# Performance work log

Hardware: AMD Instinct MI355X
Metric: run time of the kernel (lower is better)

Reference implementation:

```python
import jax, jax.numpy as jnp
import numpy as np
from jax import lax

# --- static config (Detectron defaults, C4-style RPN) ---
B, A_NUM, H, W = 8, 15, 100, 168
STRIDE = 8.0                 # 1.0 / spatial_scale
PRE_NMS = 2000               # RPN_PRE_NMS_TOP_N
POST_NMS = 1000              # RPN_POST_NMS_TOP_N
NMS_THRESH = 0.7
MIN_SIZE = 0.0
BBOX_XFORM_CLIP = float(np.log(1000.0 / 16.0))


def _make_anchors():
    sizes = np.array([32., 64., 128., 256., 512.])
    ratios = np.array([0.5, 1.0, 2.0])
    out = []
    for s in sizes:
        for r in ratios:
            w = s * np.sqrt(1.0 / r)
            h = s * np.sqrt(r)
            out.append([-(w - 1) / 2., -(h - 1) / 2., (w - 1) / 2., (h - 1) / 2.])
    return np.asarray(out, dtype=np.float32)  # [15, 4]


def setup_inputs() -> dict:
    key = jax.random.key(0)
    k1, k2 = jax.random.split(key)
    rpn_cls_prob = jax.random.uniform(k1, (B, A_NUM, H, W), jnp.float32)
    rpn_bbox_pred = jax.random.normal(k2, (B, 4 * A_NUM, H, W), jnp.float32) * 0.1
    im_info = jnp.tile(jnp.array([[H * STRIDE, W * STRIDE, 1.0]], jnp.float32), (B, 1))
    anchors = jnp.asarray(_make_anchors())
    return {"rpn_cls_prob": rpn_cls_prob, "rpn_bbox_pred": rpn_bbox_pred,
            "im_info": im_info, "anchors": anchors}


def _bbox_transform(anchors, deltas):
    # Detectron bbox_transform with weights (1,1,1,1)
    ws = anchors[:, 2] - anchors[:, 0] + 1.0
    hs = anchors[:, 3] - anchors[:, 1] + 1.0
    cx = anchors[:, 0] + 0.5 * ws
    cy = anchors[:, 1] + 0.5 * hs
    dx, dy = deltas[:, 0], deltas[:, 1]
    dw = jnp.minimum(deltas[:, 2], BBOX_XFORM_CLIP)
    dh = jnp.minimum(deltas[:, 3], BBOX_XFORM_CLIP)
    pcx = dx * ws + cx
    pcy = dy * hs + cy
    pw = jnp.exp(dw) * ws
    ph = jnp.exp(dh) * hs
    return jnp.stack([pcx - 0.5 * pw, pcy - 0.5 * ph,
                      pcx + 0.5 * pw - 1.0, pcy + 0.5 * ph - 1.0], axis=1)


def _nms_keep(boxes, valid, thresh):
    # Greedy NMS on score-sorted boxes, fixed-shape via lax.scan.
    P = boxes.shape[0]
    x1, y1, x2, y2 = boxes[:, 0], boxes[:, 1], boxes[:, 2], boxes[:, 3]
    areas = (x2 - x1 + 1.0) * (y2 - y1 + 1.0)
    iw = jnp.maximum(jnp.minimum(x2[:, None], x2[None, :]) - jnp.maximum(x1[:, None], x1[None, :]) + 1.0, 0.0)
    ih = jnp.maximum(jnp.minimum(y2[:, None], y2[None, :]) - jnp.maximum(y1[:, None], y1[None, :]) + 1.0, 0.0)
    inter = iw * ih
    iou = inter / (areas[:, None] + areas[None, :] - inter)  # [P, P]
    idxs = jnp.arange(P)

    def step(suppressed, inp):
        row, is_valid, i = inp
        keep_i = is_valid & (~suppressed[i])
        suppressed = suppressed | (keep_i & (row > thresh) & (idxs > i))
        return suppressed, keep_i

    _, keep = lax.scan(step, jnp.zeros((P,), bool), (iou, valid, idxs))
    return keep


def _one_image(scores, deltas, iminfo, all_anchors):
    # scores: [A,H,W], deltas: [4A,H,W] -> flat (h, w, a) ordering, matching
    # all_anchors built as (K, A) with K = h*W + w.
    scores_f = jnp.transpose(scores, (1, 2, 0)).reshape(-1)          # [K*A]
    deltas_f = jnp.transpose(deltas, (1, 2, 0)).reshape(-1, 4)       # [K*A, 4]
    top_s, top_i = lax.top_k(scores_f, PRE_NMS)
    props = _bbox_transform(all_anchors[top_i], deltas_f[top_i])
    # clip_tiled_boxes to image bounds
    wmax, hmax = iminfo[1] - 1.0, iminfo[0] - 1.0
    x1 = jnp.clip(props[:, 0], 0.0, wmax)
    y1 = jnp.clip(props[:, 1], 0.0, hmax)
    x2 = jnp.clip(props[:, 2], 0.0, wmax)
    y2 = jnp.clip(props[:, 3], 0.0, hmax)
    props = jnp.stack([x1, y1, x2, y2], axis=1)
    # _filter_boxes (mask instead of drop, for fixed shapes)
    ws = x2 - x1 + 1.0
    hs = y2 - y1 + 1.0
    ms = MIN_SIZE * iminfo[2]
    valid = (ws >= ms) & (hs >= ms) & ((x1 + ws / 2.0) < iminfo[1]) & ((y1 + hs / 2.0) < iminfo[0])
    keep = _nms_keep(props, valid, NMS_THRESH)
    # kept boxes first (stable sort preserves descending-score order), take POST_NMS
    order = jnp.argsort(jnp.where(keep, 0, 1).astype(jnp.int32))[:POST_NMS]
    kept = keep[order]
    boxes = jnp.where(kept[:, None], props[order], 0.0)
    probs = jnp.where(kept, top_s[order], 0.0)
    return boxes, probs


def reference(rpn_cls_prob, rpn_bbox_pred, im_info, anchors):
    shift_x = jnp.arange(W, dtype=jnp.float32) * STRIDE
    shift_y = jnp.arange(H, dtype=jnp.float32) * STRIDE
    sx, sy = jnp.meshgrid(shift_x, shift_y)                 # [H, W] each
    shifts = jnp.stack([sx.ravel(), sy.ravel(), sx.ravel(), sy.ravel()], axis=1)  # [K, 4]
    all_anchors = (anchors[None, :, :] + shifts[:, None, :]).reshape(-1, 4)       # [K*A, 4]
    boxes, probs = jax.vmap(_one_image, in_axes=(0, 0, 0, None))(
        rpn_cls_prob, rpn_bbox_pred, im_info, all_anchors)      # [B,P,4], [B,P]
    binds = jnp.broadcast_to(jnp.arange(B, dtype=jnp.float32)[:, None, None], (B, POST_NMS, 1))
    rois = jnp.concatenate([binds, boxes], axis=2).reshape(B * POST_NMS, 5)
    return rois, probs.reshape(-1)
```

## Files before the change

### kernel.cpp

```cpp
#include <hip/hip_runtime.h>
#include <hip/hip_bf16.h>
#include <math.h>

#define BN 8
#define AN 15
#define HH 100
#define WW 168
#define HW (HH*WW)
#define NPI (AN*HW)
#define NTOT (BN*NPI)
#define PRE 2000
#define POST 1000
#define CAP 4096
#define ROWW 32
#define NCHUNK 32
#define RSTRIDE 2048
#define EPB 4096
#define HBLK 62
#define GELEM 2048
#define GBLK 124

typedef unsigned int u32;
typedef unsigned long long u64;

#define OFF_H1     0
#define OFF_H2     507904
#define OFF_CSTAR  1015808
#define OFF_CCNT   1016832
#define OFF_THR    1017856
#define OFF_CAND   1018880
#define OFF_BOX    1281024
#define OFF_SCORE  1543168
#define OFF_VALID  1608704
#define OFF_MASK   1674240
#define OFF_DIAG   5868544

__device__ __forceinline__ u32 fmono(float s) {
  u32 u = __float_as_uint(s);
  return (u & 0x80000000u) ? ~u : (u | 0x80000000u);
}
__device__ __forceinline__ float funmono(u32 m) {
  u32 u = (m & 0x80000000u) ? (m ^ 0x80000000u) : ~m;
  return __uint_as_float(u);
}
__device__ __forceinline__ float areaf(float4 bx) {
  return __fmul_rn(__fadd_rn(__fsub_rn(bx.z, bx.x), 1.0f),
                   __fadd_rn(__fsub_rn(bx.w, bx.y), 1.0f));
}

#define BAR_LGKM() asm volatile("s_waitcnt lgkmcnt(0)\ns_barrier" ::: "memory")
#define WAVE_FENCE() asm volatile("" ::: "memory")

__device__ __forceinline__ u32 wave_suffix_incl(u32 v, int lane) {
  for (int d = 1; d < 64; d <<= 1) {
    u32 n = (u32)__shfl_down((int)v, d, 64);
    if (lane + d < 64) v += n;
  }
  return v;
}

__global__ __launch_bounds__(256) void hist1_kernel(const float* __restrict__ cls,
                                                    u32* __restrict__ h1) {
  __shared__ u32 lh[16 * 258];
  int b = blockIdx.y;
  int t = threadIdx.x;
  for (int q = t; q < 16 * 258; q += 256) lh[q] = 0u;
  __syncthreads();
  int start = blockIdx.x * EPB;
  int end = min(start + EPB, NPI);
  const float* p = cls + (size_t)b * NPI;
  u32 copy = ((u32)t & 15u) * 258u;
  for (int i = start + t; i < end; i += 256) {
    u32 m = fmono(p[i]);
    atomicAdd(&lh[copy + (m >> 24)], 1u);
  }
  __syncthreads();
  u32 s = 0;
#pragma unroll
  for (int cpy = 0; cpy < 16; ++cpy) s += lh[cpy * 258 + t];
  h1[((size_t)(b * HBLK) + blockIdx.x) * 256 + t] = s;
}

__global__ __launch_bounds__(256) void coarse_kernel(const u32* __restrict__ h1,
                                                     u32* __restrict__ cstar) {
  int b = blockIdx.x;
  int t = threadIdx.x;
  __shared__ u32 cnts[256];
  u32 s = 0;
  for (int blk = 0; blk < HBLK; ++blk) s += h1[((size_t)(b * HBLK) + blk) * 256 + t];
  cnts[t] = s;
  __syncthreads();
  if (t < 64) {
    int lane = t;
    u32 v0 = cnts[4 * lane + 0], v1 = cnts[4 * lane + 1];
    u32 v2 = cnts[4 * lane + 2], v3 = cnts[4 * lane + 3];
    u32 ls3 = v3, ls2 = v2 + ls3, ls1 = v1 + ls2, ls0 = v0 + ls1;
    u32 incl = wave_suffix_incl(ls0, lane);
    u32 tail = incl - ls0;
    u32 s0 = tail + ls0, s1 = tail + ls1, s2 = tail + ls2, s3 = tail + ls3;
    u32 e0 = 4 * (u32)lane;
    if (lane == 0 && s0 < (u32)PRE) { cstar[b * 32] = 0u; cstar[b * 32 + 1] = s1; }
    if (s0 >= (u32)PRE && s1 < (u32)PRE) { cstar[b * 32] = e0 + 0; cstar[b * 32 + 1] = s1; }
    if (s1 >= (u32)PRE && s2 < (u32)PRE) { cstar[b * 32] = e0 + 1; cstar[b * 32 + 1] = s2; }
    if (s2 >= (u32)PRE && s3 < (u32)PRE) { cstar[b * 32] = e0 + 2; cstar[b * 32 + 1] = s3; }
    if (s3 >= (u32)PRE && (e0 + 3 == 255u || tail < (u32)PRE)) {
      cstar[b * 32] = e0 + 3;
      cstar[b * 32 + 1] = (e0 + 3 == 255u) ? 0u : tail;
    }
  }
}

__global__ __launch_bounds__(256) void hist2_kernel(const float* __restrict__ cls,
                                                    const u32* __restrict__ cstar,
                                                    u32* __restrict__ h2) {
  __shared__ u32 lh[4 * 260];
  int b = blockIdx.y;
  int t = threadIdx.x;
  for (int q = t; q < 4 * 260; q += 256) lh[q] = 0u;
  __syncthreads();
  u32 cs = cstar[b * 32];
  int start = blockIdx.x * EPB;
  int end = min(start + EPB, NPI);
  const float* p = cls + (size_t)b * NPI;
  u32 copy = ((u32)t & 3u) * 260u;
  for (int i = start + t; i < end; i += 256) {
    u32 m = fmono(p[i]);
    if ((m >> 24) == cs) atomicAdd(&lh[copy + ((m >> 16) & 0xFFu)], 1u);
  }
  __syncthreads();
  u32 s = 0;
#pragma unroll
  for (int cpy = 0; cpy < 4; ++cpy) s += lh[cpy * 260 + t];
  h2[((size_t)(b * HBLK) + blockIdx.x) * 256 + t] = s;
}

__global__ __launch_bounds__(256) void fine_kernel(const u32* __restrict__ h2,
                                                   const u32* __restrict__ cstar,
                                                   u32* __restrict__ thr,
                                                   u32* __restrict__ ccnt) {
  int b = blockIdx.x;
  int t = threadIdx.x;
  __shared__ u32 cnts[256];
  u32 s = 0;
  for (int blk = 0; blk < HBLK; ++blk) s += h2[((size_t)(b * HBLK) + blk) * 256 + t];
  cnts[t] = s;
  __syncthreads();
  if (t == 64) ccnt[b * 32] = 0u;
  if (t < 64) {
    int lane = t;
    u32 cs = cstar[b * 32], base = cstar[b * 32 + 1];
    u32 v0 = cnts[4 * lane + 0], v1 = cnts[4 * lane + 1];
    u32 v2 = cnts[4 * lane + 2], v3 = cnts[4 * lane + 3];
    u32 ls3 = v3, ls2 = v2 + ls3, ls1 = v1 + ls2, ls0 = v0 + ls1;
    u32 incl = wave_suffix_incl(ls0, lane);
    u32 tail = incl - ls0;
    u32 s0 = base + tail + ls0, s1 = base + tail + ls1;
    u32 s2 = base + tail + ls2, s3 = base + tail + ls3;
    u32 sn = base + tail;
    u32 e0 = 4 * (u32)lane;
    if (lane == 0 && s0 < (u32)PRE) thr[b * 32] = (cs << 8);
    if (s0 >= (u32)PRE && s1 < (u32)PRE) thr[b * 32] = (cs << 8) | (e0 + 0);
    if (s1 >= (u32)PRE && s2 < (u32)PRE) thr[b * 32] = (cs << 8) | (e0 + 1);
    if (s2 >= (u32)PRE && s3 < (u32)PRE) thr[b * 32] = (cs << 8) | (e0 + 2);
    if (s3 >= (u32)PRE && (e0 + 3 == 255u || sn < (u32)PRE)) thr[b * 32] = (cs << 8) | (e0 + 3);
  }
}

__global__ __launch_bounds__(256) void gather_kernel(
    const float* __restrict__ cls, const u32* __restrict__ thr,
    u32* __restrict__ ccnt, u64* __restrict__ cand) {
  int b = blockIdx.y;
  int t = threadIdx.x;
  int lane = t & 63, wid = t >> 6;
  int base_i = blockIdx.x * GELEM;
  const float* p = cls + (size_t)b * NPI;
  u32 T = thr[b * 32];
  __shared__ int wsum[4];
  __shared__ int wbase[4];
  __shared__ u32 baseSh;

  u32 mv[8];
  u32 flags = 0;
#pragma unroll
  for (int k = 0; k < 8; ++k) {
    int i = base_i + k * 256 + t;
    u32 m = 0;
    bool ok = false;
    if (i < NPI) { m = fmono(p[i]); ok = (m >> 16) >= T; }
    mv[k] = m;
    flags |= ok ? (1u << k) : 0u;
  }
  int ct = (int)__popc(flags);
  int inc = ct;
  for (int d = 1; d < 64; d <<= 1) {
    int n = __shfl_up(inc, d, 64);
    if (lane >= d) inc += n;
  }
  int excl = inc - ct;
  if (lane == 63) wsum[wid] = inc;
  __syncthreads();
  if (t == 0) {
    int acc = 0;
#pragma unroll
    for (int w = 0; w < 4; ++w) { wbase[w] = acc; acc += wsum[w]; }
    baseSh = acc ? atomicAdd(&ccnt[b * 32], (u32)acc) : 0u;
  }
  __syncthreads();
  if (!flags) return;
  u32 pos0 = baseSh + (u32)wbase[wid] + (u32)excl;
#pragma unroll
  for (int k = 0; k < 8; ++k) {
    if ((flags >> k) & 1u) {
      u32 pos = pos0 + (u32)__popc(flags & ((1u << k) - 1u));
      if (pos < CAP) {
        int i = base_i + k * 256 + t;
        int a = i / HW;
        int hw = i - a * HW;
        u32 ti = (u32)(hw * AN + a);
        cand[(size_t)b * CAP + pos] = ((u64)mv[k] << 32) | (u32)(~ti);
      }
    }
  }
}

__global__ __launch_bounds__(1024) void sort_transform_kernel(
    const u64* __restrict__ cand, const u32* __restrict__ ccnt,
    const u32* __restrict__ thr,
    const float* __restrict__ bbox, const float* __restrict__ iminfo,
    const float* __restrict__ anch,
    float4* __restrict__ boxes, float* __restrict__ scores, int* __restrict__ valid) {
  __shared__ u64 keys[CAP];
  __shared__ u64 keys2[2048];
  __shared__ u32 h24[256];
  __shared__ u32 aboveSh, cmpCnt, t24Sh, cnt2Sh;
  int b = blockIdx.x;
  int t = threadIdx.x;
  int lane = t & 63;
  u32 cnt = ccnt[b * 32];
  if (cnt > CAP) cnt = CAP;
  u32 thr16v = thr[b * 32];
  for (int q = t; q < CAP; q += 1024) keys[q] = (q < (int)cnt) ? cand[(size_t)b * CAP + q] : 0ULL;
  keys2[t] = 0ULL; keys2[t + 1024] = 0ULL;
  if (t < 256) h24[t] = 0u;
  if (t == 0) { aboveSh = 0u; cmpCnt = 0u; }
  __syncthreads();

  for (int q0 = 0; q0 < CAP; q0 += 1024) {
    int q = q0 + t;
    u64 key = keys[q];
    u32 hi = (u32)(key >> 32);
    bool isReal = (q < (int)cnt);
    bool above = isReal && ((hi >> 16) > thr16v);
    u64 bal = __ballot(above);
    if (lane == 0 && bal) atomicAdd(&aboveSh, (u32)__popcll(bal));
    if (isReal && !above) atomicAdd(&h24[(hi >> 8) & 0xFFu], 1u);
  }
  __syncthreads();
  if (t < 64) {
    u32 basev = aboveSh;
    u32 v0 = h24[4 * lane + 0], v1 = h24[4 * lane + 1];
    u32 v2 = h24[4 * lane + 2], v3 = h24[4 * lane + 3];
    u32 ls3 = v3, ls2 = v2 + ls3, ls1 = v1 + ls2, ls0 = v0 + ls1;
    u32 incl = wave_suffix_incl(ls0, lane);
    u32 tail = incl - ls0;
    u32 s0 = basev + tail + ls0, s1 = basev + tail + ls1;
    u32 s2 = basev + tail + ls2, s3 = basev + tail + ls3;
    u32 sn = basev + tail;
    u32 e0 = 4 * (u32)lane;
    if (lane == 0 && s0 < (u32)PRE) { t24Sh = 0u; cnt2Sh = s0; }
    if (s0 >= (u32)PRE && s1 < (u32)PRE) { t24Sh = e0 + 0; cnt2Sh = s0; }
    if (s1 >= (u32)PRE && s2 < (u32)PRE) { t24Sh = e0 + 1; cnt2Sh = s1; }
    if (s2 >= (u32)PRE && s3 < (u32)PRE) { t24Sh = e0 + 2; cnt2Sh = s2; }
    if (s3 >= (u32)PRE && (e0 + 3 == 255u || sn < (u32)PRE)) { t24Sh = e0 + 3; cnt2Sh = s3; }
  }
  __syncthreads();
  u32 cnt2 = cnt2Sh;
  bool fallback = (cnt2 > 2048u);

  if (!fallback) {
    u32 t24 = (thr16v << 8) | t24Sh;
    for (int q0 = 0; q0 < CAP; q0 += 1024) {
      int q = q0 + t;
      u64 key = keys[q];
      u32 hi = (u32)(key >> 32);
      bool pass = (q < (int)cnt) && ((hi >> 8) >= t24);
      u64 bal = __ballot(pass);
      if (bal) {
        u32 wb = 0;
        if (lane == 0) wb = atomicAdd(&cmpCnt, (u32)__popcll(bal));
        wb = (u32)__shfl((int)wb, 0, 64);
        if (pass) {
          u32 rank = (u32)__popcll(bal & ((1ULL << lane) - 1ULL));
          keys2[wb + rank] = key;
        }
      }
    }
    __syncthreads();
    for (u32 k = 2; k <= 2048; k <<= 1) {
      for (u32 j = k >> 1; j > 0; j >>= 1) {
        bool cross = (j >= 128);
        if (cross) __syncthreads();
        u32 idx = (u32)t;
        u32 base2 = ((idx & ~(j - 1)) << 1) | (idx & (j - 1));
        u32 partner = base2 + j;
        bool up2 = ((base2 & k) == 0);
        u64 A = keys2[base2], Bv = keys2[partner];
        bool sw = up2 ? (A < Bv) : (A > Bv);
        if (sw) { keys2[base2] = Bv; keys2[partner] = A; }
        if (cross) { if (j == 128) __syncthreads(); }
        else WAVE_FENCE();
      }
    }
    __syncthreads();
  } else {
    for (u32 k = 2; k <= CAP; k <<= 1) {
      for (u32 j = k >> 1; j > 0; j >>= 1) {
        for (int p = 0; p < CAP / 2 / 1024; ++p) {
          u32 idx = (u32)t + (u32)p * 1024u;
          u32 base2 = ((idx & ~(j - 1)) << 1) | (idx & (j - 1));
          u32 partner = base2 + j;
          bool up2 = ((base2 & k) == 0);
          u64 A = keys[base2], Bv = keys[partner];
          bool sw = up2 ? (A < Bv) : (A > Bv);
          if (sw) { keys[base2] = Bv; keys[partner] = A; }
        }
        __syncthreads();
      }
    }
  }

  float im_h = iminfo[b * 3 + 0], im_w = iminfo[b * 3 + 1], im_s = iminfo[b * 3 + 2];
  float wmax = __fsub_rn(im_w, 1.0f), hmax = __fsub_rn(im_h, 1.0f);
  float msz = __fmul_rn(0.0f, im_s);
  const float BCLIP = (float)4.135166556742356;
  for (int q = t; q < PRE; q += 1024) {
    u64 key = fallback ? keys[q] : keys2[q];
    u32 i = ~((u32)key);
    if (q >= (int)cnt || i >= (u32)NPI) {
      boxes[b * RSTRIDE + q] = make_float4(0.f, 0.f, 0.f, 0.f);
      scores[b * RSTRIDE + q] = 0.f;
      valid[b * RSTRIDE + q] = 0;
      continue;
    }
    float sc = funmono((u32)(key >> 32));
    int a = (int)(i % AN);
    int pp = (int)(i / AN);
    int w = pp % WW;
    int h = pp / WW;
    float sx = (float)(w * 8), sy = (float)(h * 8);
    float ax1 = __fadd_rn(anch[a * 4 + 0], sx);
    float ay1 = __fadd_rn(anch[a * 4 + 1], sy);
    float ax2 = __fadd_rn(anch[a * 4 + 2], sx);
    float ay2 = __fadd_rn(anch[a * 4 + 3], sy);
    float wsA = __fadd_rn(__fsub_rn(ax2, ax1), 1.0f);
    float hsA = __fadd_rn(__fsub_rn(ay2, ay1), 1.0f);
    float cx = __fadd_rn(ax1, __fmul_rn(0.5f, wsA));
    float cy = __fadd_rn(ay1, __fmul_rn(0.5f, hsA));
    const float* dp = bbox + ((size_t)b * (4 * AN) + 4 * a) * HW + (size_t)h * WW + w;
    float dx = dp[0], dy = dp[HW], dwv = dp[2 * HW], dhv = dp[3 * HW];
    dwv = fminf(dwv, BCLIP);
    dhv = fminf(dhv, BCLIP);
    float pcx = __fadd_rn(__fmul_rn(dx, wsA), cx);
    float pcy = __fadd_rn(__fmul_rn(dy, hsA), cy);
    float pw = __fmul_rn((float)exp((double)dwv), wsA);
    float ph = __fmul_rn((float)exp((double)dhv), hsA);
    float hpw = __fmul_rn(0.5f, pw), hph = __fmul_rn(0.5f, ph);
    float x1 = __fsub_rn(pcx, hpw);
    float y1 = __fsub_rn(pcy, hph);
    float x2 = __fsub_rn(__fadd_rn(pcx, hpw), 1.0f);
    float y2 = __fsub_rn(__fadd_rn(pcy, hph), 1.0f);
    x1 = fminf(fmaxf(x1, 0.0f), wmax);
    y1 = fminf(fmaxf(y1, 0.0f), hmax);
    x2 = fminf(fmaxf(x2, 0.0f), wmax);
    y2 = fminf(fmaxf(y2, 0.0f), hmax);
    float ws2 = __fadd_rn(__fsub_rn(x2, x1), 1.0f);
    float hs2 = __fadd_rn(__fsub_rn(y2, y1), 1.0f);
    int v = (ws2 >= msz) && (hs2 >= msz) &&
            (__fadd_rn(x1, __fmul_rn(ws2, 0.5f)) < im_w) &&
            (__fadd_rn(y1, __fmul_rn(hs2, 0.5f)) < im_h);
    boxes[b * RSTRIDE + q] = make_float4(x1, y1, x2, y2);
    scores[b * RSTRIDE + q] = sc;
    valid[b * RSTRIDE + q] = v;
  }
}

__global__ __launch_bounds__(64) void nms_mask_kernel(const float4* __restrict__ boxes,
                                                      u64* __restrict__ mask,
                                                      u64* __restrict__ diag) {
  int L = blockIdx.x, b = blockIdx.y;
  int ib = 0, rowlen = 32;
  while (L >= rowlen) { L -= rowlen; rowlen--; ib++; }
  int jb = ib + L;
  int t = threadIdx.x;
  __shared__ float4 jbox[64];
  __shared__ float jarea[64];
  int jbase = jb * 64;
  int jcount = min(64, PRE - jbase);
  if (t < jcount) {
    float4 bj = boxes[b * RSTRIDE + jbase + t];
    jbox[t] = bj;
    jarea[t] = areaf(bj);
  }
  __syncthreads();
  int i = ib * 64 + t;
  if (i >= PRE) return;
  float4 bi = boxes[b * RSTRIDE + i];
  float ai = areaf(bi);
  u64 word = 0ULL;
  for (int jj = 0; jj < jcount; ++jj) {
    int j = jbase + jj;
    if (j <= i) continue;
    float4 bj = jbox[jj];
    float iw = fmaxf(__fadd_rn(__fsub_rn(fminf(bi.z, bj.z), fmaxf(bi.x, bj.x)), 1.0f), 0.0f);
    float ih = fmaxf(__fadd_rn(__fsub_rn(fminf(bi.w, bj.w), fmaxf(bi.y, bj.y)), 1.0f), 0.0f);
    float inter = __fmul_rn(iw, ih);
    float denom = __fsub_rn(__fadd_rn(ai, jarea[jj]), inter);
    float iou = inter / denom;
    if (iou > 0.7f) word |= (1ULL << jj);
  }
  mask[((size_t)(b * RSTRIDE) + i) * ROWW + jb] = word;
  if (jb == ib) diag[(size_t)b * RSTRIDE + i] = word;
}

__global__ __launch_bounds__(512) void seq_nms_kernel(
    const u64* __restrict__ mask, const u64* __restrict__ diag,
    const int* __restrict__ valid,
    const float4* __restrict__ boxes, const float* __restrict__ scores,
    float* __restrict__ out) {
  int b = blockIdx.x;
  int tid = threadIdx.x;
  int wid = tid >> 6, lane = tid & 63, lw = lane & 31, hf = lane >> 5;
  __shared__ u64 partial[16];
  __shared__ u64 keepbLDS;
  __shared__ u64 vbufLDS[NCHUNK];
  __shared__ u64 kbits_s[NCHUNK];
  __shared__ int chunkoff[NCHUNK];
  __shared__ int keeplist[PRE];
  __shared__ int Ksh;
  __shared__ int stopSh;

  if (tid < 16) partial[tid] = 0ULL;
  if (tid < NCHUNK) kbits_s[tid] = 0ULL;
  if (tid == 0) stopSh = 0;
  if (wid == 0) {
    for (int c = 0; c < NCHUNK; ++c) {
      int q = c * 64 + lane;
      int v = (q < PRE) ? valid[b * RSTRIDE + q] : 0;
      u64 bl = __ballot(v != 0);
      if (lane == 0) vbufLDS[c] = bl;
    }
  }
  __syncthreads();

  const u64* base = mask + (size_t)b * RSTRIDE * ROWW;
  const u64* dg = diag + (size_t)b * RSTRIDE;

  u64 rem = 0ULL;
  u64 Dv = 0ULL;
  if (wid == 0) Dv = dg[lane];
  int rb0 = wid * 8 + hf;
  int tot = 0;
  u64 cur0 = base[(size_t)(rb0 + 0) * ROWW + lw];
  u64 cur1 = base[(size_t)(rb0 + 2) * ROWW + lw];
  u64 cur2 = base[(size_t)(rb0 + 4) * ROWW + lw];
  u64 cur3 = base[(size_t)(rb0 + 6) * ROWW + lw];
  for (int c = 0; c < NCHUNK; ++c) {
    u64 n0 = 0, n1 = 0, n2 = 0, n3 = 0, Dnext = 0ULL;
    if (c + 1 < NCHUNK) {
      int c0n = (c + 1) * 64;
      n0 = base[(size_t)(c0n + rb0 + 0) * ROWW + lw];
      n1 = base[(size_t)(c0n + rb0 + 2) * ROWW + lw];
      n2 = base[(size_t)(c0n + rb0 + 4) * ROWW + lw];
      n3 = base[(size_t)(c0n + rb0 + 6) * ROWW + lw];
      if (wid == 0) Dnext = dg[(size_t)(c + 1) * 64 + lane];
    }
    if (wid == 0) {
      u64 nz = __ballot(Dv != 0ULL);
      u64 cv = partial[0];
#pragma unroll
      for (int s = 1; s < 16; ++s) cv |= partial[s];
      u32 clo = (u32)__builtin_amdgcn_readfirstlane((int)(u32)cv);
      u32 chi = (u32)__builtin_amdgcn_readfirstlane((int)(u32)(cv >> 32));
      u64 cl = ((u64)chi << 32) | clo;
      u64 vbv = vbufLDS[c];
      u32 vlo = (u32)__builtin_amdgcn_readfirstlane((int)(u32)vbv);
      u32 vhi = (u32)__builtin_amdgcn_readfirstlane((int)(u32)(vbv >> 32));
      u64 vb = ((u64)vhi << 32) | vlo;
      u32 dloA = (u32)Dv, dhiA = (u32)(Dv >> 32);
      u64 work = nz & vb;
      while (work) {
        int ii = __builtin_ctzll(work);
        work &= work - 1ULL;
        u32 dlo = (u32)__builtin_amdgcn_readlane((int)dloA, ii);
        u32 dhi = (u32)__builtin_amdgcn_readlane((int)dhiA, ii);
        u64 D = ((u64)dhi << 32) | dlo;
        u64 tt = ((~cl & vb) >> ii) & 1ULL;
        cl |= tt ? D : 0ULL;
      }
      u64 keepb = vb & ~cl;
      tot += (int)__popcll(keepb);
      if (lane == 0) {
        keepbLDS = keepb;
        kbits_s[c] = keepb;
        if (tot >= POST) stopSh = 1;
      }
    }
    BAR_LGKM();
    u64 keepb = keepbLDS;
    int stop = stopSh;
    rem |= cur0 & (0ULL - ((keepb >> (rb0 + 0)) & 1ULL));
    rem |= cur1 & (0ULL - ((keepb >> (rb0 + 2)) & 1ULL));
    rem |= cur2 & (0ULL - ((keepb >> (rb0 + 4)) & 1ULL));
    rem |= cur3 & (0ULL - ((keepb >> (rb0 + 6)) & 1ULL));
    int nw = (c + 1) & 31;
    if (lw == nw) partial[wid * 2 + hf] = rem;
    if (stop) break;
    BAR_LGKM();
    cur0 = n0; cur1 = n1; cur2 = n2; cur3 = n3;
    Dv = Dnext;
  }
  __syncthreads();

  if (wid == 0) {
    int pc = (lane < NCHUNK) ? (int)__popcll(kbits_s[lane]) : 0;
    int inc = pc;
    for (int d = 1; d < 64; d <<= 1) {
      int n = __shfl_up(inc, d, 64);
      if (lane >= d) inc += n;
    }
    if (lane < NCHUNK) chunkoff[lane] = inc - pc;
    if (lane == NCHUNK - 1) Ksh = inc;
  }
  __syncthreads();
  for (int c = wid * 4; c < wid * 4 + 4; ++c) {
    u64 word = kbits_s[c];
    if ((word >> lane) & 1ULL) {
      int rank = (int)__popcll(word & ((1ULL << lane) - 1ULL));
      keeplist[chunkoff[c] + rank] = c * 64 + lane;
    }
  }
  __syncthreads();
  int K = Ksh;

  float* rois = out;
  float* probs = out + (size_t)BN * POST * 5;
  for (int r = tid; r < POST; r += 512) {
    float x1 = 0.f, y1 = 0.f, x2 = 0.f, y2 = 0.f, pr = 0.f;
    if (r < K) {
      int i = keeplist[r];
      float4 bb = boxes[b * RSTRIDE + i];
      x1 = bb.x; y1 = bb.y; x2 = bb.z; y2 = bb.w;
      pr = scores[b * RSTRIDE + i];
    }
    size_t ro = (size_t)(b * POST + r) * 5;
    rois[ro + 0] = (float)b;
    rois[ro + 1] = x1; rois[ro + 2] = y1; rois[ro + 3] = x2; rois[ro + 4] = y2;
    probs[b * POST + r] = pr;
  }
}

extern "C" void kernel_launch(void* const* d_in, const int* in_sizes, int n_in,
                              void* d_out, int out_size, void* d_ws, size_t ws_size,
                              hipStream_t stream) {
  const float* cls    = (const float*)d_in[0];
  const float* bbox   = (const float*)d_in[1];
  const float* iminfo = (const float*)d_in[2];
  const float* anch   = (const float*)d_in[3];
  char* ws = (char*)d_ws;
  u32* h1    = (u32*)(ws + OFF_H1);
  u32* h2    = (u32*)(ws + OFF_H2);
  u32* cstar = (u32*)(ws + OFF_CSTAR);
  u32* ccnt  = (u32*)(ws + OFF_CCNT);
  u32* thr   = (u32*)(ws + OFF_THR);
  u64* cand  = (u64*)(ws + OFF_CAND);
  float4* boxes = (float4*)(ws + OFF_BOX);
  float* scores = (float*)(ws + OFF_SCORE);
  int* valid    = (int*)(ws + OFF_VALID);
  u64* mask     = (u64*)(ws + OFF_MASK);
  u64* diag     = (u64*)(ws + OFF_DIAG);
  float* out = (float*)d_out;

  hist1_kernel<<<dim3(HBLK, BN), 256, 0, stream>>>(cls, h1);
  coarse_kernel<<<BN, 256, 0, stream>>>(h1, cstar);
  hist2_kernel<<<dim3(HBLK, BN), 256, 0, stream>>>(cls, cstar, h2);
  fine_kernel<<<BN, 256, 0, stream>>>(h2, cstar, thr, ccnt);
  gather_kernel<<<dim3(GBLK, BN), 256, 0, stream>>>(cls, thr, ccnt, cand);
  sort_transform_kernel<<<BN, 1024, 0, stream>>>(cand, ccnt, thr, bbox, iminfo, anch,
                                                 boxes, scores, valid);
  nms_mask_kernel<<<dim3(528, BN), 64, 0, stream>>>(boxes, mask, diag);
  seq_nms_kernel<<<BN, 512, 0, stream>>>(mask, diag, valid, boxes, scores, out);
}
```

Baseline: 182.4 us.

## Sort candidates in registers with shuffle bitonic stages; vectorize histogram and gather loads

The 2048-key bitonic sort in sort_transform_kernel now keeps two keys per thread in registers. Strides under 128 use 64-bit wave shuffles or an in-thread compare instead of shared-memory exchanges, and the box transform is applied straight from registers. Separately, the hist1, hist2 and gather kernels read scores as float4 on full blocks, and gather remaps candidate indices to match. This cuts LDS traffic and barriers in the sort and issues fewer, wider global loads, at the cost of more code paths and index-remapping complexity.

```diff
diff --git a/kernel.cpp b/kernel.cpp
--- a/kernel.cpp
+++ b/kernel.cpp
@@ -49,7 +49,6 @@
 }
 
 #define BAR_LGKM() asm volatile("s_waitcnt lgkmcnt(0)\ns_barrier" ::: "memory")
-#define WAVE_FENCE() asm volatile("" ::: "memory")
 
 __device__ __forceinline__ u32 wave_suffix_incl(u32 v, int lane) {
   for (int d = 1; d < 64; d <<= 1) {
@@ -57,6 +56,10 @@
     if (lane + d < 64) v += n;
   }
   return v;
+}
+
+__device__ __forceinline__ u64 shfl_xor64(u64 v, int m) {
+  return (u64)__shfl_xor((unsigned long long)v, m, 64);
 }
 
 __global__ __launch_bounds__(256) void hist1_kernel(const float* __restrict__ cls,
@@ -67,12 +70,24 @@
   for (int q = t; q < 16 * 258; q += 256) lh[q] = 0u;
   __syncthreads();
   int start = blockIdx.x * EPB;
-  int end = min(start + EPB, NPI);
   const float* p = cls + (size_t)b * NPI;
   u32 copy = ((u32)t & 15u) * 258u;
-  for (int i = start + t; i < end; i += 256) {
-    u32 m = fmono(p[i]);
-    atomicAdd(&lh[copy + (m >> 24)], 1u);
+  if (start + EPB <= NPI) {
+    const float4* p4 = (const float4*)(p + start);
+#pragma unroll
+    for (int q = 0; q < 4; ++q) {
+      float4 v = p4[q * 256 + t];
+      atomicAdd(&lh[copy + (fmono(v.x) >> 24)], 1u);
+      atomicAdd(&lh[copy + (fmono(v.y) >> 24)], 1u);
+      atomicAdd(&lh[copy + (fmono(v.z) >> 24)], 1u);
+      atomicAdd(&lh[copy + (fmono(v.w) >> 24)], 1u);
+    }
+  } else {
+    int end = NPI;
+    for (int i = start + t; i < end; i += 256) {
+      u32 m = fmono(p[i]);
+      atomicAdd(&lh[copy + (m >> 24)], 1u);
+    }
   }
   __syncthreads();
   u32 s = 0;
@@ -120,12 +135,25 @@
   __syncthreads();
   u32 cs = cstar[b * 32];
   int start = blockIdx.x * EPB;
-  int end = min(start + EPB, NPI);
   const float* p = cls + (size_t)b * NPI;
   u32 copy = ((u32)t & 3u) * 260u;
-  for (int i = start + t; i < end; i += 256) {
-    u32 m = fmono(p[i]);
-    if ((m >> 24) == cs) atomicAdd(&lh[copy + ((m >> 16) & 0xFFu)], 1u);
+  if (start + EPB <= NPI) {
+    const float4* p4 = (const float4*)(p + start);
+#pragma unroll
+    for (int q = 0; q < 4; ++q) {
+      float4 v = p4[q * 256 + t];
+      u32 m;
+      m = fmono(v.x); if ((m >> 24) == cs) atomicAdd(&lh[copy + ((m >> 16) & 0xFFu)], 1u);
+      m = fmono(v.y); if ((m >> 24) == cs) atomicAdd(&lh[copy + ((m >> 16) & 0xFFu)], 1u);
+      m = fmono(v.z); if ((m >> 24) == cs) atomicAdd(&lh[copy + ((m >> 16) & 0xFFu)], 1u);
+      m = fmono(v.w); if ((m >> 24) == cs) atomicAdd(&lh[copy + ((m >> 16) & 0xFFu)], 1u);
+    }
+  } else {
+    int end = NPI;
+    for (int i = start + t; i < end; i += 256) {
+      u32 m = fmono(p[i]);
+      if ((m >> 24) == cs) atomicAdd(&lh[copy + ((m >> 16) & 0xFFu)], 1u);
+    }
   }
   __syncthreads();
   u32 s = 0;
@@ -181,14 +209,34 @@
 
   u32 mv[8];
   u32 flags = 0;
-#pragma unroll
-  for (int k = 0; k < 8; ++k) {
-    int i = base_i + k * 256 + t;
-    u32 m = 0;
-    bool ok = false;
-    if (i < NPI) { m = fmono(p[i]); ok = (m >> 16) >= T; }
-    mv[k] = m;
-    flags |= ok ? (1u << k) : 0u;
+  bool vec = (base_i + GELEM <= NPI);
+  if (vec) {
+    const float4* p4 = (const float4*)(p + base_i);
+    float4 a = p4[t], c = p4[256 + t];
+#pragma unroll
+    for (int k = 0; k < 4; ++k) {
+      float vv = (k == 0) ? a.x : (k == 1) ? a.y : (k == 2) ? a.z : a.w;
+      u32 m = fmono(vv);
+      mv[k] = m;
+      flags |= ((m >> 16) >= T) ? (1u << k) : 0u;
+    }
+#pragma unroll
+    for (int k = 0; k < 4; ++k) {
+      float vv = (k == 0) ? c.x : (k == 1) ? c.y : (k == 2) ? c.z : c.w;
+      u32 m = fmono(vv);
+      mv[4 + k] = m;
+      flags |= ((m >> 16) >= T) ? (1u << (4 + k)) : 0u;
+    }
+  } else {
+#pragma unroll
+    for (int k = 0; k < 8; ++k) {
+      int i = base_i + k * 256 + t;
+      u32 m = 0;
+      bool ok = false;
+      if (i < NPI) { m = fmono(p[i]); ok = (m >> 16) >= T; }
+      mv[k] = m;
+      flags |= ok ? (1u << k) : 0u;
+    }
   }
   int ct = (int)__popc(flags);
   int inc = ct;
@@ -213,7 +261,8 @@
     if ((flags >> k) & 1u) {
       u32 pos = pos0 + (u32)__popc(flags & ((1u << k) - 1u));
       if (pos < CAP) {
-        int i = base_i + k * 256 + t;
+        int i = vec ? (base_i + (k < 4 ? 4 * t + k : 1024 + 4 * t + (k - 4)))
+                    : (base_i + k * 256 + t);
         int a = i / HW;
         int hw = i - a * HW;
         u32 ti = (u32)(hw * AN + a);
@@ -221,6 +270,60 @@
       }
     }
   }
+}
+
+__device__ __forceinline__ void transform_one(
+    u64 key, int q, int b, u32 cnt,
+    float im_h, float im_w, float wmax, float hmax, float msz,
+    const float* __restrict__ bbox, const float* __restrict__ anch,
+    float4* __restrict__ boxes, float* __restrict__ scores, int* __restrict__ valid) {
+  const float BCLIP = (float)4.135166556742356;
+  u32 i = ~((u32)key);
+  if (q >= (int)cnt || i >= (u32)NPI) {
+    boxes[b * RSTRIDE + q] = make_float4(0.f, 0.f, 0.f, 0.f);
+    scores[b * RSTRIDE + q] = 0.f;
+    valid[b * RSTRIDE + q] = 0;
+    return;
+  }
+  float sc = funmono((u32)(key >> 32));
+  int a = (int)(i % AN);
+  int pp = (int)(i / AN);
+  int w = pp % WW;
+  int h = pp / WW;
+  float sx = (float)(w * 8), sy = (float)(h * 8);
+  float ax1 = __fadd_rn(anch[a * 4 + 0], sx);
+  float ay1 = __fadd_rn(anch[a * 4 + 1], sy);
+  float ax2 = __fadd_rn(anch[a * 4 + 2], sx);
+  float ay2 = __fadd_rn(anch[a * 4 + 3], sy);
+  float wsA = __fadd_rn(__fsub_rn(ax2, ax1), 1.0f);
+  float hsA = __fadd_rn(__fsub_rn(ay2, ay1), 1.0f);
+  float cx = __fadd_rn(ax1, __fmul_rn(0.5f, wsA));
+  float cy = __fadd_rn(ay1, __fmul_rn(0.5f, hsA));
+  const float* dp = bbox + ((size_t)b * (4 * AN) + 4 * a) * HW + (size_t)h * WW + w;
+  float dx = dp[0], dy = dp[HW], dwv = dp[2 * HW], dhv = dp[3 * HW];
+  dwv = fminf(dwv, BCLIP);
+  dhv = fminf(dhv, BCLIP);
+  float pcx = __fadd_rn(__fmul_rn(dx, wsA), cx);
+  float pcy = __fadd_rn(__fmul_rn(dy, hsA), cy);
+  float pw = __fmul_rn((float)exp((double)dwv), wsA);
+  float ph = __fmul_rn((float)exp((double)dhv), hsA);
+  float hpw = __fmul_rn(0.5f, pw), hph = __fmul_rn(0.5f, ph);
+  float x1 = __fsub_rn(pcx, hpw);
+  float y1 = __fsub_rn(pcy, hph);
+  float x2 = __fsub_rn(__fadd_rn(pcx, hpw), 1.0f);
+  float y2 = __fsub_rn(__fadd_rn(pcy, hph), 1.0f);
+  x1 = fminf(fmaxf(x1, 0.0f), wmax);
+  y1 = fminf(fmaxf(y1, 0.0f), hmax);
+  x2 = fminf(fmaxf(x2, 0.0f), wmax);
+  y2 = fminf(fmaxf(y2, 0.0f), hmax);
+  float ws2 = __fadd_rn(__fsub_rn(x2, x1), 1.0f);
+  float hs2 = __fadd_rn(__fsub_rn(y2, y1), 1.0f);
+  int v = (ws2 >= msz) && (hs2 >= msz) &&
+          (__fadd_rn(x1, __fmul_rn(ws2, 0.5f)) < im_w) &&
+          (__fadd_rn(y1, __fmul_rn(hs2, 0.5f)) < im_h);
+  boxes[b * RSTRIDE + q] = make_float4(x1, y1, x2, y2);
+  scores[b * RSTRIDE + q] = sc;
+  valid[b * RSTRIDE + q] = v;
 }
 
 __global__ __launch_bounds__(1024) void sort_transform_kernel(
@@ -277,6 +380,10 @@
   u32 cnt2 = cnt2Sh;
   bool fallback = (cnt2 > 2048u);
 
+  float im_h = iminfo[b * 3 + 0], im_w = iminfo[b * 3 + 1], im_s = iminfo[b * 3 + 2];
+  float wmax = __fsub_rn(im_w, 1.0f), hmax = __fsub_rn(im_h, 1.0f);
+  float msz = __fmul_rn(0.0f, im_s);
+
   if (!fallback) {
     u32 t24 = (thr16v << 8) | t24Sh;
     for (int q0 = 0; q0 < CAP; q0 += 1024) {
@@ -296,22 +403,42 @@
       }
     }
     __syncthreads();
+    u64 e0 = keys2[2 * t], e1 = keys2[2 * t + 1];
     for (u32 k = 2; k <= 2048; k <<= 1) {
-      for (u32 j = k >> 1; j > 0; j >>= 1) {
-        bool cross = (j >= 128);
-        if (cross) __syncthreads();
-        u32 idx = (u32)t;
-        u32 base2 = ((idx & ~(j - 1)) << 1) | (idx & (j - 1));
-        u32 partner = base2 + j;
-        bool up2 = ((base2 & k) == 0);
-        u64 A = keys2[base2], Bv = keys2[partner];
-        bool sw = up2 ? (A < Bv) : (A > Bv);
-        if (sw) { keys2[base2] = Bv; keys2[partner] = A; }
-        if (cross) { if (j == 128) __syncthreads(); }
-        else WAVE_FENCE();
+      u32 kb = k >> 1;
+      for (u32 j = k >> 1; j >= 1; j >>= 1) {
+        bool up = ((u32)t & kb) == 0;
+        if (j >= 128) {
+          keys2[2 * t] = e0; keys2[2 * t + 1] = e1;
+          __syncthreads();
+          int pt = t ^ (int)(j >> 1);
+          u64 y0 = keys2[2 * pt], y1 = keys2[2 * pt + 1];
+          bool low = ((u32)t & (j >> 1)) == 0;
+          bool mx = (up == low);
+          e0 = mx ? (e0 > y0 ? e0 : y0) : (e0 < y0 ? e0 : y0);
+          e1 = mx ? (e1 > y1 ? e1 : y1) : (e1 < y1 ? e1 : y1);
+          __syncthreads();
+        } else if (j >= 2) {
+          int m = (int)(j >> 1);
+          u64 y0 = shfl_xor64(e0, m), y1 = shfl_xor64(e1, m);
+          bool low = ((u32)t & (u32)m) == 0;
+          bool mx = (up == low);
+          e0 = mx ? (e0 > y0 ? e0 : y0) : (e0 < y0 ? e0 : y0);
+          e1 = mx ? (e1 > y1 ? e1 : y1) : (e1 < y1 ? e1 : y1);
+        } else {
+          u64 mx64 = (e0 > e1) ? e0 : e1;
+          u64 mn64 = (e0 > e1) ? e1 : e0;
+          e0 = up ? mx64 : mn64;
+          e1 = up ? mn64 : mx64;
+        }
       }
     }
-    __syncthreads();
+    if (2 * t < PRE) {
+      transform_one(e0, 2 * t, b, cnt, im_h, im_w, wmax, hmax, msz,
+                    bbox, anch, boxes, scores, valid);
+      transform_one(e1, 2 * t + 1, b, cnt, im_h, im_w, wmax, hmax, msz,
+                    bbox, anch, boxes, scores, valid);
+    }
   } else {
     for (u32 k = 2; k <= CAP; k <<= 1) {
       for (u32 j = k >> 1; j > 0; j >>= 1) {
@@ -327,60 +454,9 @@
         __syncthreads();
       }
     }
-  }
-
-  float im_h = iminfo[b * 3 + 0], im_w = iminfo[b * 3 + 1], im_s = iminfo[b * 3 + 2];
-  float wmax = __fsub_rn(im_w, 1.0f), hmax = __fsub_rn(im_h, 1.0f);
-  float msz = __fmul_rn(0.0f, im_s);
-  const float BCLIP = (float)4.135166556742356;
-  for (int q = t; q < PRE; q += 1024) {
-    u64 key = fallback ? keys[q] : keys2[q];
-    u32 i = ~((u32)key);
-    if (q >= (int)cnt || i >= (u32)NPI) {
-      boxes[b * RSTRIDE + q] = make_float4(0.f, 0.f, 0.f, 0.f);
-      scores[b * RSTRIDE + q] = 0.f;
-      valid[b * RSTRIDE + q] = 0;
-      continue;
-    }
-    float sc = funmono((u32)(key >> 32));
-    int a = (int)(i % AN);
-    int pp = (int)(i / AN);
-    int w = pp % WW;
-    int h = pp / WW;
-    float sx = (float)(w * 8), sy = (float)(h * 8);
-    float ax1 = __fadd_rn(anch[a * 4 + 0], sx);
-    float ay1 = __fadd_rn(anch[a * 4 + 1], sy);
-    float ax2 = __fadd_rn(anch[a * 4 + 2], sx);
-    float ay2 = __fadd_rn(anch[a * 4 + 3], sy);
-    float wsA = __fadd_rn(__fsub_rn(ax2, ax1), 1.0f);
-    float hsA = __fadd_rn(__fsub_rn(ay2, ay1), 1.0f);
-    float cx = __fadd_rn(ax1, __fmul_rn(0.5f, wsA));
-    float cy = __fadd_rn(ay1, __fmul_rn(0.5f, hsA));
-    const float* dp = bbox + ((size_t)b * (4 * AN) + 4 * a) * HW + (size_t)h * WW + w;
-    float dx = dp[0], dy = dp[HW], dwv = dp[2 * HW], dhv = dp[3 * HW];
-    dwv = fminf(dwv, BCLIP);
-    dhv = fminf(dhv, BCLIP);
-    float pcx = __fadd_rn(__fmul_rn(dx, wsA), cx);
-    float pcy = __fadd_rn(__fmul_rn(dy, hsA), cy);
-    float pw = __fmul_rn((float)exp((double)dwv), wsA);
-    float ph = __fmul_rn((float)exp((double)dhv), hsA);
-    float hpw = __fmul_rn(0.5f, pw), hph = __fmul_rn(0.5f, ph);
-    float x1 = __fsub_rn(pcx, hpw);
-    float y1 = __fsub_rn(pcy, hph);
-    float x2 = __fsub_rn(__fadd_rn(pcx, hpw), 1.0f);
-    float y2 = __fsub_rn(__fadd_rn(pcy, hph), 1.0f);
-    x1 = fminf(fmaxf(x1, 0.0f), wmax);
-    y1 = fminf(fmaxf(y1, 0.0f), hmax);
-    x2 = fminf(fmaxf(x2, 0.0f), wmax);
-    y2 = fminf(fmaxf(y2, 0.0f), hmax);
-    float ws2 = __fadd_rn(__fsub_rn(x2, x1), 1.0f);
-    float hs2 = __fadd_rn(__fsub_rn(y2, y1), 1.0f);
-    int v = (ws2 >= msz) && (hs2 >= msz) &&
-            (__fadd_rn(x1, __fmul_rn(ws2, 0.5f)) < im_w) &&
-            (__fadd_rn(y1, __fmul_rn(hs2, 0.5f)) < im_h);
-    boxes[b * RSTRIDE + q] = make_float4(x1, y1, x2, y2);
-    scores[b * RSTRIDE + q] = sc;
-    valid[b * RSTRIDE + q] = v;
+    for (int q = t; q < PRE; q += 1024)
+      transform_one(keys[q], q, b, cnt, im_h, im_w, wmax, hmax, msz,
+                    bbox, anch, boxes, scores, valid);
   }
 }
 
```

Result: faster. 177.7 us (-2.6%).
